# Kernel optimization log

Hardware: AMD Instinct MI355X
Metric: run time of the kernel (lower is better)

The kernel has to match this reference:

```python
import jax, jax.numpy as jnp
import numpy as np

B, S, D_DIM = 32, 512, 1024

def setup_inputs() -> dict:
    key = jax.random.key(0)
    k1, k2, k3, k4 = jax.random.split(key, 4)
    return {
        "D": jax.random.normal(k1, (B, S, D_DIM), dtype=jnp.float32),
        "H": jax.random.normal(k2, (B, S, D_DIM), dtype=jnp.float32),
        # learned params: U is (d+1, d) (xavier-style scale), W is (2d+1,)
        # (original inits W to zeros; we use small random values so the linear
        #  term is exercised — same math either way)
        "U": jax.random.normal(k3, (D_DIM + 1, D_DIM), dtype=jnp.float32) * 0.02,
        "W": jax.random.normal(k4, (2 * D_DIM + 1,), dtype=jnp.float32) * 0.02,
    }

def reference(D, H, U, W):
    # D, H: [B, S, d]; U: [d+1, d]; W: [2d+1]
    d = H.shape[-1]
    ones = jnp.ones(D.shape[:2] + (1,), dtype=D.dtype)
    Daug = jnp.concatenate([D, ones], axis=-1)              # [B, S, d+1]
    # bilinear term: v.U.u  -> [B, Sx, Sy]
    bil = jnp.einsum('bxi,ij,byj->bxy', Daug, U, H)
    # linear term W . concat(D_aug, H): algebraically split — avoids the
    # O(B*S*S*2d) concatenated intermediate of the original implementation
    lin = (Daug @ W[:d + 1])[:, :, None] + (H @ W[d + 1:])[:, None, :]
    return bil + lin
```

## Files before the change

### kernel.cpp

```cpp
#include <hip/hip_runtime.h>


#define D_DIM 1024
#define ROWS 16384

typedef float floatx4 __attribute__((ext_vector_type(4)));
typedef __bf16 bf16x8 __attribute__((ext_vector_type(8)));

__device__ inline unsigned short f2bf(float f) {
  unsigned int u = __builtin_bit_cast(unsigned int, f);
  u = (u + 0x7FFFu + ((u >> 16) & 1u)) >> 16;
  return (unsigned short)u;
}

__device__ inline void async_load16(const void* g, void* l) {
  __builtin_amdgcn_global_load_lds(
      (const __attribute__((address_space(1))) void*)g,
      (__attribute__((address_space(3))) void*)l, 16, 0, 0);
}

__global__ __launch_bounds__(256) void prep_kernel(
    const float* __restrict__ D, const float* __restrict__ H,
    const float* __restrict__ U, const float* __restrict__ W,
    unsigned short* __restrict__ Dbf, unsigned short* __restrict__ Hbf,
    unsigned short* __restrict__ Ut, float* __restrict__ Ubias,
    float* __restrict__ linD) {
  __shared__ float tile[32][33];
  int bid = blockIdx.x;
  int tid = threadIdx.x;
  if (bid < 8192) {
    bool isH = bid >= 4096;
    int wave = tid >> 6, lane = tid & 63;
    int r = ((isH ? bid - 4096 : bid) << 2) + wave;
    const float* src = (isH ? H : D) + (size_t)r * D_DIM;
    unsigned short* dst = (isH ? Hbf : Dbf) + (size_t)r * D_DIM;
    float s = 0.f;
    #pragma unroll
    for (int i = 0; i < 4; ++i) {
      int c = lane + 64 * i;
      float4 v = ((const float4*)src)[c];
      ushort4 o;
      o.x = f2bf(v.x); o.y = f2bf(v.y); o.z = f2bf(v.z); o.w = f2bf(v.w);
      ((ushort4*)dst)[c] = o;
      if (!isH) {
        float4 wv = ((const float4*)W)[c];
        s += v.x * wv.x + v.y * wv.y + v.z * wv.z + v.w * wv.w;
      }
    }
    if (!isH) {
      #pragma unroll
      for (int off = 32; off > 0; off >>= 1) s += __shfl_down(s, off, 64);
      if (lane == 0) linD[r] = s + W[D_DIM];
    }
  } else if (bid < 9216) {
    int t = bid - 8192;
    int n0 = (t & 31) * 32, k0 = (t >> 5) * 32;
    int tr = tid >> 5, tc = tid & 31;
    #pragma unroll
    for (int i = 0; i < 32; i += 8)
      tile[tr + i][tc] = U[(size_t)(k0 + tr + i) * D_DIM + n0 + tc];
    __syncthreads();
    #pragma unroll
    for (int i = 0; i < 32; i += 8)
      Ut[(size_t)(n0 + tr + i) * D_DIM + k0 + tc] = f2bf(tile[tc][tr + i]);
  } else {
    int j = (bid - 9216) * 256 + tid;
    Ubias[j] = U[(size_t)D_DIM * D_DIM + j] + W[D_DIM + 1 + j];
  }
}

__device__ inline void gemm_core_swz(
    const unsigned short* __restrict__ A, const unsigned short* __restrict__ Bt,
    int m0, int n0, unsigned short* As, unsigned short* Bs,
    floatx4 (&acc)[4][4]) {
  const int K = D_DIM;
  int tid = threadIdx.x;
  int l = tid & 63, wave = tid >> 6;
  int quad = l >> 4, lrow = l & 15;
  int wm = wave >> 1, wn = wave & 1;

  int srow = 8 * wave + (l >> 3);
  int sq = (l & 7) ^ (l >> 3);
  const unsigned short* gA = A + (size_t)(m0 + srow) * K + sq * 8;
  const unsigned short* gB = Bt + (size_t)(n0 + srow) * K + sq * 8;

  int rl = lrow & 7, gofs = lrow >> 3;
  int baseA = wm * 512 + gofs * 64 + rl * 8;
  int baseB = wn * 512 + gofs * 64 + rl * 8;

  for (int k0 = 0; k0 < K; k0 += 64) {
    __syncthreads();
    #pragma unroll
    for (int j = 0; j < 4; ++j) {
      async_load16(gA + (size_t)(32 * j) * K + k0, As + (j * 256 + tid) * 8);
      async_load16(gB + (size_t)(32 * j) * K + k0, Bs + (j * 256 + tid) * 8);
    }
    __syncthreads();
    #pragma unroll
    for (int s = 0; s < 2; ++s) {
      int xq = (s * 4 + quad) ^ rl;
      bf16x8 a[4], b[4];
      #pragma unroll
      for (int mt = 0; mt < 4; ++mt)
        a[mt] = *(const bf16x8*)(As + (baseA + mt * 128 + xq) * 8);
      #pragma unroll
      for (int nt = 0; nt < 4; ++nt)
        b[nt] = *(const bf16x8*)(Bs + (baseB + nt * 128 + xq) * 8);
      #pragma unroll
      for (int mt = 0; mt < 4; ++mt)
        #pragma unroll
        for (int nt = 0; nt < 4; ++nt)
          acc[mt][nt] = __builtin_amdgcn_mfma_f32_16x16x32_bf16(
              a[mt], b[nt], acc[mt][nt], 0, 0, 0);
    }
  }
}

__global__ __launch_bounds__(256) void gemm1_kernel(
    const unsigned short* __restrict__ A,
    const unsigned short* __restrict__ Bt,
    const float* __restrict__ Ubias,
    unsigned short* __restrict__ T) {
  __shared__ __align__(16) unsigned short As[128 * 64];
  __shared__ __align__(16) unsigned short Bs[128 * 64];
  int m0 = blockIdx.x * 128, n0 = blockIdx.y * 128;
  int tid = threadIdx.x;
  int lane = tid & 63, wave = tid >> 6;
  int quad = lane >> 4, lrow = lane & 15;
  int wm = wave >> 1, wn = wave & 1;

  floatx4 acc[4][4] = {};
  gemm_core_swz(A, Bt, m0, n0, As, Bs, acc);

  #pragma unroll
  for (int mt = 0; mt < 4; ++mt)
    #pragma unroll
    for (int nt = 0; nt < 4; ++nt) {
      int row = m0 + wm * 64 + mt * 16 + quad * 4;
      int col = n0 + wn * 64 + nt * 16 + lrow;
      float bias = Ubias[col];
      #pragma unroll
      for (int rr = 0; rr < 4; ++rr)
        T[(size_t)(row + rr) * D_DIM + col] = f2bf(acc[mt][nt][rr] + bias);
    }
}

__global__ __launch_bounds__(256) void gemm2_kernel(
    const unsigned short* __restrict__ Tg,
    const unsigned short* __restrict__ Hbf,
    const float* __restrict__ linD,
    float* __restrict__ out) {
  __shared__ __align__(16) unsigned short As[128 * 64];
  __shared__ __align__(16) unsigned short Bs[128 * 64];
  int b = blockIdx.x;
  int t = blockIdx.y;
  int m0 = (t >> 2) * 128, n0 = (t & 3) * 128;
  const unsigned short* A = Tg + (size_t)b * 512 * D_DIM;
  const unsigned short* Bt = Hbf + (size_t)b * 512 * D_DIM;
  int tid = threadIdx.x;
  int lane = tid & 63, wave = tid >> 6;
  int quad = lane >> 4, lrow = lane & 15;
  int wm = wave >> 1, wn = wave & 1;

  floatx4 acc[4][4] = {};
  gemm_core_swz(A, Bt, m0, n0, As, Bs, acc);

  #pragma unroll
  for (int mt = 0; mt < 4; ++mt)
    #pragma unroll
    for (int nt = 0; nt < 4; ++nt) {
      int row = m0 + wm * 64 + mt * 16 + quad * 4;
      int col = n0 + wn * 64 + nt * 16 + lrow;
      #pragma unroll
      for (int rr = 0; rr < 4; ++rr) {
        float v = acc[mt][nt][rr] + linD[b * 512 + row + rr];
        out[((size_t)b * 512 + row + rr) * 512 + col] = v;
      }
    }
}

extern "C" void kernel_launch(void* const* d_in, const int* in_sizes, int n_in,
                              void* d_out, int out_size, void* d_ws, size_t ws_size,
                              hipStream_t stream) {
  const float* D = (const float*)d_in[0];
  const float* H = (const float*)d_in[1];
  const float* U = (const float*)d_in[2];
  const float* W = (const float*)d_in[3];
  float* out = (float*)d_out;

  char* ws = (char*)d_ws;
  unsigned short* Dbf = (unsigned short*)ws; ws += (size_t)ROWS * D_DIM * 2;
  unsigned short* Hbf = (unsigned short*)ws; ws += (size_t)ROWS * D_DIM * 2;
  unsigned short* Tbf = (unsigned short*)ws; ws += (size_t)ROWS * D_DIM * 2;
  unsigned short* Ut  = (unsigned short*)ws; ws += (size_t)D_DIM * D_DIM * 2;
  float* Ubias = (float*)ws;                 ws += (size_t)D_DIM * 4;
  float* linD = (float*)ws;                  ws += (size_t)ROWS * 4;

  prep_kernel<<<dim3(9220), 256, 0, stream>>>(D, H, U, W, Dbf, Hbf, Ut, Ubias, linD);
  gemm1_kernel<<<dim3(128, 8), 256, 0, stream>>>(Dbf, Ut, Ubias, Tbf);
  gemm2_kernel<<<dim3(32, 16), 256, 0, stream>>>(Tbf, Hbf, linD, out);
}
```

Before: 229.4 us.

## Move H bf16 conversion into gemm1 launch to overlap with GEMM work

```diff
diff --git a/kernel.cpp b/kernel.cpp
--- a/kernel.cpp
+++ b/kernel.cpp
@@ -20,40 +20,29 @@
 }
 
 __global__ __launch_bounds__(256) void prep_kernel(
-    const float* __restrict__ D, const float* __restrict__ H,
-    const float* __restrict__ U, const float* __restrict__ W,
-    unsigned short* __restrict__ Dbf, unsigned short* __restrict__ Hbf,
-    unsigned short* __restrict__ Ut, float* __restrict__ Ubias,
-    float* __restrict__ linD) {
+    const float* __restrict__ D, const float* __restrict__ U,
+    const float* __restrict__ W,
+    unsigned short* __restrict__ Dbf, unsigned short* __restrict__ Ut,
+    float* __restrict__ Ubias, float* __restrict__ linD) {
   __shared__ float tile[32][33];
+  __shared__ float red[4];
   int bid = blockIdx.x;
   int tid = threadIdx.x;
-  if (bid < 8192) {
-    bool isH = bid >= 4096;
-    int wave = tid >> 6, lane = tid & 63;
-    int r = ((isH ? bid - 4096 : bid) << 2) + wave;
-    const float* src = (isH ? H : D) + (size_t)r * D_DIM;
-    unsigned short* dst = (isH ? Hbf : Dbf) + (size_t)r * D_DIM;
-    float s = 0.f;
-    #pragma unroll
-    for (int i = 0; i < 4; ++i) {
-      int c = lane + 64 * i;
-      float4 v = ((const float4*)src)[c];
-      ushort4 o;
-      o.x = f2bf(v.x); o.y = f2bf(v.y); o.z = f2bf(v.z); o.w = f2bf(v.w);
-      ((ushort4*)dst)[c] = o;
-      if (!isH) {
-        float4 wv = ((const float4*)W)[c];
-        s += v.x * wv.x + v.y * wv.y + v.z * wv.z + v.w * wv.w;
-      }
-    }
-    if (!isH) {
-      #pragma unroll
-      for (int off = 32; off > 0; off >>= 1) s += __shfl_down(s, off, 64);
-      if (lane == 0) linD[r] = s + W[D_DIM];
-    }
-  } else if (bid < 9216) {
-    int t = bid - 8192;
+  if (bid < ROWS) {
+    const float* src = D + (size_t)bid * D_DIM;
+    float4 v = ((const float4*)src)[tid];
+    float4 wv = ((const float4*)W)[tid];
+    ushort4 o;
+    o.x = f2bf(v.x); o.y = f2bf(v.y); o.z = f2bf(v.z); o.w = f2bf(v.w);
+    ((ushort4*)(Dbf + (size_t)bid * D_DIM))[tid] = o;
+    float s = v.x * wv.x + v.y * wv.y + v.z * wv.z + v.w * wv.w;
+    #pragma unroll
+    for (int off = 32; off > 0; off >>= 1) s += __shfl_down(s, off, 64);
+    if ((tid & 63) == 0) red[tid >> 6] = s;
+    __syncthreads();
+    if (tid == 0) linD[bid] = red[0] + red[1] + red[2] + red[3] + W[D_DIM];
+  } else if (bid < ROWS + 1024) {
+    int t = bid - ROWS;
     int n0 = (t & 31) * 32, k0 = (t >> 5) * 32;
     int tr = tid >> 5, tc = tid & 31;
     #pragma unroll
@@ -64,7 +53,7 @@
     for (int i = 0; i < 32; i += 8)
       Ut[(size_t)(n0 + tr + i) * D_DIM + k0 + tc] = f2bf(tile[tc][tr + i]);
   } else {
-    int j = (bid - 9216) * 256 + tid;
+    int j = (bid - ROWS - 1024) * 256 + tid;
     Ubias[j] = U[(size_t)D_DIM * D_DIM + j] + W[D_DIM + 1 + j];
   }
 }
@@ -120,11 +109,22 @@
     const unsigned short* __restrict__ A,
     const unsigned short* __restrict__ Bt,
     const float* __restrict__ Ubias,
-    unsigned short* __restrict__ T) {
+    unsigned short* __restrict__ T,
+    const float* __restrict__ H,
+    unsigned short* __restrict__ Hbf) {
   __shared__ __align__(16) unsigned short As[128 * 64];
   __shared__ __align__(16) unsigned short Bs[128 * 64];
-  int m0 = blockIdx.x * 128, n0 = blockIdx.y * 128;
-  int tid = threadIdx.x;
+  int bid = blockIdx.x;
+  int tid = threadIdx.x;
+  if (bid >= 1024) {
+    int r = bid - 1024;
+    float4 v = ((const float4*)(H + (size_t)r * D_DIM))[tid];
+    ushort4 o;
+    o.x = f2bf(v.x); o.y = f2bf(v.y); o.z = f2bf(v.z); o.w = f2bf(v.w);
+    ((ushort4*)(Hbf + (size_t)r * D_DIM))[tid] = o;
+    return;
+  }
+  int m0 = (bid & 127) * 128, n0 = (bid >> 7) * 128;
   int lane = tid & 63, wave = tid >> 6;
   int quad = lane >> 4, lrow = lane & 15;
   int wm = wave >> 1, wn = wave & 1;
@@ -196,7 +196,7 @@
   float* Ubias = (float*)ws;                 ws += (size_t)D_DIM * 4;
   float* linD = (float*)ws;                  ws += (size_t)ROWS * 4;
 
-  prep_kernel<<<dim3(9220), 256, 0, stream>>>(D, H, U, W, Dbf, Hbf, Ut, Ubias, linD);
-  gemm1_kernel<<<dim3(128, 8), 256, 0, stream>>>(Dbf, Ut, Ubias, Tbf);
+  prep_kernel<<<dim3(ROWS + 1024 + 4), 256, 0, stream>>>(D, U, W, Dbf, Ut, Ubias, linD);
+  gemm1_kernel<<<dim3(1024 + ROWS), 256, 0, stream>>>(Dbf, Ut, Ubias, Tbf, H, Hbf);
   gemm2_kernel<<<dim3(32, 16), 256, 0, stream>>>(Tbf, Hbf, linD, out);
 }
```

Result: no change. 231.8 us (+1.0%).

## Fuse D/H conversion, both GEMMs into one persistent kernel with per-batch flags

Applied to the files above, without the earlier changes.

```diff
diff --git a/kernel.cpp b/kernel.cpp
--- a/kernel.cpp
+++ b/kernel.cpp
@@ -1,4 +1,5 @@
 #include <hip/hip_runtime.h>
+#include <hip/hip_bf16.h>
 
 
 #define D_DIM 1024
@@ -19,42 +20,23 @@
       (__attribute__((address_space(3))) void*)l, 16, 0, 0);
 }
 
+__device__ inline bf16x8 cvt8(float4 a, float4 b) {
+  union { bf16x8 v; __hip_bfloat162 h[4]; } u;
+  u.h[0] = __float22bfloat162_rn(make_float2(a.x, a.y));
+  u.h[1] = __float22bfloat162_rn(make_float2(a.z, a.w));
+  u.h[2] = __float22bfloat162_rn(make_float2(b.x, b.y));
+  u.h[3] = __float22bfloat162_rn(make_float2(b.z, b.w));
+  return u.v;
+}
+
 __global__ __launch_bounds__(256) void prep_kernel(
-    const float* __restrict__ D, const float* __restrict__ H,
     const float* __restrict__ U, const float* __restrict__ W,
-    unsigned short* __restrict__ Dbf, unsigned short* __restrict__ Hbf,
     unsigned short* __restrict__ Ut, float* __restrict__ Ubias,
-    float* __restrict__ linD) {
+    int* __restrict__ flags) {
   __shared__ float tile[32][33];
-  int bid = blockIdx.x;
-  int tid = threadIdx.x;
-  if (bid < 8192) {
-    bool isH = bid >= 4096;
-    int wave = tid >> 6, lane = tid & 63;
-    int r = ((isH ? bid - 4096 : bid) << 2) + wave;
-    const float* src = (isH ? H : D) + (size_t)r * D_DIM;
-    unsigned short* dst = (isH ? Hbf : Dbf) + (size_t)r * D_DIM;
-    float s = 0.f;
-    #pragma unroll
-    for (int i = 0; i < 4; ++i) {
-      int c = lane + 64 * i;
-      float4 v = ((const float4*)src)[c];
-      ushort4 o;
-      o.x = f2bf(v.x); o.y = f2bf(v.y); o.z = f2bf(v.z); o.w = f2bf(v.w);
-      ((ushort4*)dst)[c] = o;
-      if (!isH) {
-        float4 wv = ((const float4*)W)[c];
-        s += v.x * wv.x + v.y * wv.y + v.z * wv.z + v.w * wv.w;
-      }
-    }
-    if (!isH) {
-      #pragma unroll
-      for (int off = 32; off > 0; off >>= 1) s += __shfl_down(s, off, 64);
-      if (lane == 0) linD[r] = s + W[D_DIM];
-    }
-  } else if (bid < 9216) {
-    int t = bid - 8192;
-    int n0 = (t & 31) * 32, k0 = (t >> 5) * 32;
+  int bid = blockIdx.x, tid = threadIdx.x;
+  if (bid < 1024) {
+    int n0 = (bid & 31) * 32, k0 = (bid >> 5) * 32;
     int tr = tid >> 5, tc = tid & 31;
     #pragma unroll
     for (int i = 0; i < 32; i += 8)
@@ -63,120 +45,213 @@
     #pragma unroll
     for (int i = 0; i < 32; i += 8)
       Ut[(size_t)(n0 + tr + i) * D_DIM + k0 + tc] = f2bf(tile[tc][tr + i]);
+  } else if (bid < 1028) {
+    int j = (bid - 1024) * 256 + tid;
+    Ubias[j] = U[(size_t)D_DIM * D_DIM + j] + W[D_DIM + 1 + j];
   } else {
-    int j = (bid - 9216) * 256 + tid;
-    Ubias[j] = U[(size_t)D_DIM * D_DIM + j] + W[D_DIM + 1 + j];
-  }
-}
-
-__device__ inline void gemm_core_swz(
-    const unsigned short* __restrict__ A, const unsigned short* __restrict__ Bt,
-    int m0, int n0, unsigned short* As, unsigned short* Bs,
-    floatx4 (&acc)[4][4]) {
-  const int K = D_DIM;
-  int tid = threadIdx.x;
-  int l = tid & 63, wave = tid >> 6;
+    if (tid < 32) flags[tid] = 0;
+  }
+}
+
+__device__ inline void stage_u(const unsigned short* __restrict__ Ut,
+                               char* buf, int tid, int it) {
+  int nc = it >> 4, kc = it & 15;
+  #pragma unroll
+  for (int i = 0; i < 4; ++i) {
+    int idx = i * 256 + tid;
+    int nl = idx >> 3, jj = idx & 7, q = jj ^ (nl & 7);
+    async_load16(Ut + (size_t)(nc * 128 + nl) * D_DIM + kc * 64 + q * 8,
+                 buf + idx * 16);
+  }
+}
+
+__device__ inline void stage_2(const unsigned short* __restrict__ Tblk,
+                               const unsigned short* __restrict__ Hbf,
+                               char* buf, int tid, int w, int l, int b, int k2) {
+  #pragma unroll
+  for (int i = 0; i < 2; ++i) {
+    int idx = i * 256 + tid;
+    int m = idx >> 3, jj = idx & 7, q = jj ^ (m & 7);
+    async_load16(Tblk + (size_t)m * D_DIM + k2 * 64 + q * 8, buf + idx * 16);
+  }
+  int q = (l & 7) ^ (l >> 3);
+  #pragma unroll
+  for (int j = 0; j < 16; ++j) {
+    int row = 32 * j + 8 * w + (l >> 3);
+    async_load16(Hbf + ((size_t)b * 512 + row) * D_DIM + k2 * 64 + q * 8,
+                 buf + 8192 + (j * 256 + tid) * 16);
+  }
+}
+
+__global__ __launch_bounds__(256, 1) void fused_kernel(
+    const float* __restrict__ D, const float* __restrict__ H,
+    const float* __restrict__ W, const unsigned short* __restrict__ Ut,
+    const float* __restrict__ Ubias, unsigned short* __restrict__ Hbf,
+    unsigned short* __restrict__ Tbf, float* __restrict__ linDg,
+    int* __restrict__ flags, float* __restrict__ out) {
+  extern __shared__ char smem[];
+  unsigned short* Dls = (unsigned short*)smem;
+  float* linD_lds = (float*)(smem + 131072);
+  char* Ub0 = smem + 131072;
+  char* Ub1 = smem + 147456;
+  int bid = blockIdx.x, tid = threadIdx.x;
+  int b = bid & 31, x = bid >> 5;
+  int l = tid & 63, w = tid >> 6;
   int quad = l >> 4, lrow = l & 15;
-  int wm = wave >> 1, wn = wave & 1;
-
-  int srow = 8 * wave + (l >> 3);
-  int sq = (l & 7) ^ (l >> 3);
-  const unsigned short* gA = A + (size_t)(m0 + srow) * K + sq * 8;
-  const unsigned short* gB = Bt + (size_t)(n0 + srow) * K + sq * 8;
-
-  int rl = lrow & 7, gofs = lrow >> 3;
-  int baseA = wm * 512 + gofs * 64 + rl * 8;
-  int baseB = wn * 512 + gofs * 64 + rl * 8;
-
-  for (int k0 = 0; k0 < K; k0 += 64) {
-    __syncthreads();
-    #pragma unroll
-    for (int j = 0; j < 4; ++j) {
-      async_load16(gA + (size_t)(32 * j) * K + k0, As + (j * 256 + tid) * 8);
-      async_load16(gB + (size_t)(32 * j) * K + k0, Bs + (j * 256 + tid) * 8);
-    }
-    __syncthreads();
+  size_t rowbase = (size_t)b * 512 + x * 64;
+
+  if (tid < 64) linD_lds[tid] = W[D_DIM];
+  __syncthreads();
+  {
+    int q = tid & 127, rh = tid >> 7;
+    float4 w0 = ((const float4*)(W + q * 8))[0];
+    float4 w1 = ((const float4*)(W + q * 8))[1];
+    #pragma unroll 4
+    for (int j = 0; j < 32; ++j) {
+      int row = 2 * j + rh;
+      const float4* src = (const float4*)(D + (rowbase + row) * D_DIM + q * 8);
+      float4 v0 = src[0], v1 = src[1];
+      *(bf16x8*)(Dls + ((size_t)row * 128 + (q ^ (row & 7))) * 8) = cvt8(v0, v1);
+      float s = v0.x * w0.x + v0.y * w0.y + v0.z * w0.z + v0.w * w0.w
+              + v1.x * w1.x + v1.y * w1.y + v1.z * w1.z + v1.w * w1.w;
+      #pragma unroll
+      for (int off = 32; off > 0; off >>= 1) s += __shfl_down(s, off, 64);
+      if (l == 0) atomicAdd(&linD_lds[row], s);
+    }
+    #pragma unroll 4
+    for (int j = 0; j < 32; ++j) {
+      int row = 2 * j + rh;
+      const float4* src = (const float4*)(H + (rowbase + row) * D_DIM + q * 8);
+      float4 v0 = src[0], v1 = src[1];
+      *(bf16x8*)(Hbf + (rowbase + row) * D_DIM + q * 8) = cvt8(v0, v1);
+    }
+  }
+  __threadfence();
+  __syncthreads();
+  if (tid == 0)
+    __hip_atomic_fetch_add(&flags[b], 1, __ATOMIC_RELEASE, __HIP_MEMORY_SCOPE_AGENT);
+  if (tid < 64) linDg[rowbase + tid] = linD_lds[tid];
+  __syncthreads();
+
+  unsigned short* Tblk = Tbf + (size_t)bid * (64 * D_DIM);
+  floatx4 acc[4][2];
+  stage_u(Ut, Ub0, tid, 0);
+  for (int it = 0; it < 128; ++it) {
+    int nc = it >> 4, kc = it & 15;
+    __syncthreads();
+    if (it + 1 < 128) stage_u(Ut, (it & 1) ? Ub0 : Ub1, tid, it + 1);
+    if (kc == 0) {
+      #pragma unroll
+      for (int mt = 0; mt < 4; ++mt)
+        #pragma unroll
+        for (int nt = 0; nt < 2; ++nt)
+          #pragma unroll
+          for (int rr = 0; rr < 4; ++rr) acc[mt][nt][rr] = 0.f;
+    }
+    unsigned short* ub = (unsigned short*)((it & 1) ? Ub1 : Ub0);
     #pragma unroll
     for (int s = 0; s < 2; ++s) {
-      int xq = (s * 4 + quad) ^ rl;
-      bf16x8 a[4], b[4];
+      int qg = kc * 8 + s * 4 + quad;
+      bf16x8 a[4], bb[2];
+      #pragma unroll
+      for (int mt = 0; mt < 4; ++mt) {
+        int m = mt * 16 + lrow;
+        a[mt] = *(const bf16x8*)(Dls + ((size_t)m * 128 + (qg ^ (m & 7))) * 8);
+      }
+      #pragma unroll
+      for (int nt = 0; nt < 2; ++nt) {
+        int nl = w * 32 + nt * 16 + lrow;
+        bb[nt] = *(const bf16x8*)(ub + ((size_t)nl * 8 + ((s * 4 + quad) ^ (nl & 7))) * 8);
+      }
       #pragma unroll
       for (int mt = 0; mt < 4; ++mt)
-        a[mt] = *(const bf16x8*)(As + (baseA + mt * 128 + xq) * 8);
-      #pragma unroll
-      for (int nt = 0; nt < 4; ++nt)
-        b[nt] = *(const bf16x8*)(Bs + (baseB + nt * 128 + xq) * 8);
+        #pragma unroll
+        for (int nt = 0; nt < 2; ++nt)
+          acc[mt][nt] = __builtin_amdgcn_mfma_f32_16x16x32_bf16(
+              a[mt], bb[nt], acc[mt][nt], 0, 0, 0);
+    }
+    if (kc == 15) {
+      #pragma unroll
+      for (int nt = 0; nt < 2; ++nt) {
+        int col = nc * 128 + w * 32 + nt * 16 + lrow;
+        float bias = Ubias[col];
+        #pragma unroll
+        for (int mt = 0; mt < 4; ++mt)
+          #pragma unroll
+          for (int rr = 0; rr < 4; ++rr)
+            Tblk[(size_t)(mt * 16 + quad * 4 + rr) * D_DIM + col] =
+                f2bf(acc[mt][nt][rr] + bias);
+      }
+    }
+  }
+  __syncthreads();
+
+  volatile int* ok = (int*)(smem + 150000);
+  if (tid == 0) {
+    int itc = 0;
+    while (__hip_atomic_load(&flags[b], __ATOMIC_ACQUIRE, __HIP_MEMORY_SCOPE_AGENT) < 8
+           && itc < 20000) { __builtin_amdgcn_s_sleep(8); ++itc; }
+    *ok = (itc < 20000) ? 1 : 0;
+  }
+  __syncthreads();
+  if (!*ok) {
+    int q = tid & 127, rh = tid >> 7;
+    for (int j = 0; j < 256; ++j) {
+      int row = 2 * j + rh;
+      const float4* src = (const float4*)(H + ((size_t)b * 512 + row) * D_DIM + q * 8);
+      float4 v0 = src[0], v1 = src[1];
+      *(bf16x8*)(Hbf + ((size_t)b * 512 + row) * D_DIM + q * 8) = cvt8(v0, v1);
+    }
+    __threadfence();
+    __syncthreads();
+  }
+
+  floatx4 acc2[4][8] = {};
+  char* Sb0 = smem;
+  char* Sb1 = smem + 73728;
+  stage_2(Tblk, Hbf, Sb0, tid, w, l, b, 0);
+  for (int k2 = 0; k2 < 16; ++k2) {
+    __syncthreads();
+    if (k2 + 1 < 16) stage_2(Tblk, Hbf, (k2 & 1) ? Sb0 : Sb1, tid, w, l, b, k2 + 1);
+    unsigned short* tb = (unsigned short*)((k2 & 1) ? Sb1 : Sb0);
+    unsigned short* hb = tb + 4096;
+    #pragma unroll
+    for (int s = 0; s < 2; ++s) {
+      int q = s * 4 + quad;
+      bf16x8 a[4], bb[8];
+      #pragma unroll
+      for (int mt = 0; mt < 4; ++mt) {
+        int m = mt * 16 + lrow;
+        a[mt] = *(const bf16x8*)(tb + ((size_t)m * 8 + (q ^ (m & 7))) * 8);
+      }
+      #pragma unroll
+      for (int yt = 0; yt < 8; ++yt) {
+        int y = w * 128 + yt * 16 + lrow;
+        bb[yt] = *(const bf16x8*)(hb + ((size_t)y * 8 + (q ^ (y & 7))) * 8);
+      }
       #pragma unroll
       for (int mt = 0; mt < 4; ++mt)
         #pragma unroll
-        for (int nt = 0; nt < 4; ++nt)
-          acc[mt][nt] = __builtin_amdgcn_mfma_f32_16x16x32_bf16(
-              a[mt], b[nt], acc[mt][nt], 0, 0, 0);
-    }
-  }
-}
-
-__global__ __launch_bounds__(256) void gemm1_kernel(
-    const unsigned short* __restrict__ A,
-    const unsigned short* __restrict__ Bt,
-    const float* __restrict__ Ubias,
-    unsigned short* __restrict__ T) {
-  __shared__ __align__(16) unsigned short As[128 * 64];
-  __shared__ __align__(16) unsigned short Bs[128 * 64];
-  int m0 = blockIdx.x * 128, n0 = blockIdx.y * 128;
-  int tid = threadIdx.x;
-  int lane = tid & 63, wave = tid >> 6;
-  int quad = lane >> 4, lrow = lane & 15;
-  int wm = wave >> 1, wn = wave & 1;
-
-  floatx4 acc[4][4] = {};
-  gemm_core_swz(A, Bt, m0, n0, As, Bs, acc);
-
-  #pragma unroll
-  for (int mt = 0; mt < 4; ++mt)
-    #pragma unroll
-    for (int nt = 0; nt < 4; ++nt) {
-      int row = m0 + wm * 64 + mt * 16 + quad * 4;
-      int col = n0 + wn * 64 + nt * 16 + lrow;
-      float bias = Ubias[col];
+        for (int yt = 0; yt < 8; ++yt)
+          acc2[mt][yt] = __builtin_amdgcn_mfma_f32_16x16x32_bf16(
+              a[mt], bb[yt], acc2[mt][yt], 0, 0, 0);
+    }
+  }
+  #pragma unroll
+  for (int mt = 0; mt < 4; ++mt) {
+    float ld[4];
+    #pragma unroll
+    for (int rr = 0; rr < 4; ++rr)
+      ld[rr] = linDg[rowbase + mt * 16 + quad * 4 + rr];
+    #pragma unroll
+    for (int yt = 0; yt < 8; ++yt) {
+      int col = w * 128 + yt * 16 + lrow;
       #pragma unroll
       for (int rr = 0; rr < 4; ++rr)
-        T[(size_t)(row + rr) * D_DIM + col] = f2bf(acc[mt][nt][rr] + bias);
-    }
-}
-
-__global__ __launch_bounds__(256) void gemm2_kernel(
-    const unsigned short* __restrict__ Tg,
-    const unsigned short* __restrict__ Hbf,
-    const float* __restrict__ linD,
-    float* __restrict__ out) {
-  __shared__ __align__(16) unsigned short As[128 * 64];
-  __shared__ __align__(16) unsigned short Bs[128 * 64];
-  int b = blockIdx.x;
-  int t = blockIdx.y;
-  int m0 = (t >> 2) * 128, n0 = (t & 3) * 128;
-  const unsigned short* A = Tg + (size_t)b * 512 * D_DIM;
-  const unsigned short* Bt = Hbf + (size_t)b * 512 * D_DIM;
-  int tid = threadIdx.x;
-  int lane = tid & 63, wave = tid >> 6;
-  int quad = lane >> 4, lrow = lane & 15;
-  int wm = wave >> 1, wn = wave & 1;
-
-  floatx4 acc[4][4] = {};
-  gemm_core_swz(A, Bt, m0, n0, As, Bs, acc);
-
-  #pragma unroll
-  for (int mt = 0; mt < 4; ++mt)
-    #pragma unroll
-    for (int nt = 0; nt < 4; ++nt) {
-      int row = m0 + wm * 64 + mt * 16 + quad * 4;
-      int col = n0 + wn * 64 + nt * 16 + lrow;
-      #pragma unroll
-      for (int rr = 0; rr < 4; ++rr) {
-        float v = acc[mt][nt][rr] + linD[b * 512 + row + rr];
-        out[((size_t)b * 512 + row + rr) * 512 + col] = v;
-      }
-    }
+        out[(rowbase + mt * 16 + quad * 4 + rr) * 512 + col] =
+            acc2[mt][yt][rr] + ld[rr];
+    }
+  }
 }
 
 extern "C" void kernel_launch(void* const* d_in, const int* in_sizes, int n_in,
@@ -189,14 +264,16 @@
   float* out = (float*)d_out;
 
   char* ws = (char*)d_ws;
-  unsigned short* Dbf = (unsigned short*)ws; ws += (size_t)ROWS * D_DIM * 2;
   unsigned short* Hbf = (unsigned short*)ws; ws += (size_t)ROWS * D_DIM * 2;
   unsigned short* Tbf = (unsigned short*)ws; ws += (size_t)ROWS * D_DIM * 2;
   unsigned short* Ut  = (unsigned short*)ws; ws += (size_t)D_DIM * D_DIM * 2;
   float* Ubias = (float*)ws;                 ws += (size_t)D_DIM * 4;
-  float* linD = (float*)ws;                  ws += (size_t)ROWS * 4;
-
-  prep_kernel<<<dim3(9220), 256, 0, stream>>>(D, H, U, W, Dbf, Hbf, Ut, Ubias, linD);
-  gemm1_kernel<<<dim3(128, 8), 256, 0, stream>>>(Dbf, Ut, Ubias, Tbf);
-  gemm2_kernel<<<dim3(32, 16), 256, 0, stream>>>(Tbf, Hbf, linD, out);
-}
+  float* linDg = (float*)ws;                 ws += (size_t)ROWS * 4;
+  int* flags   = (int*)ws;                   ws += 128;
+
+  prep_kernel<<<dim3(1029), 256, 0, stream>>>(U, W, Ut, Ubias, flags);
+  hipFuncSetAttribute((const void*)fused_kernel,
+                      hipFuncAttributeMaxDynamicSharedMemorySize, 163840);
+  fused_kernel<<<dim3(256), 256, 163840, stream>>>(
+      D, H, W, Ut, Ubias, Hbf, Tbf, linDg, flags, out);
+}
```

After: 323.7 us. 1.41x slower.

## Double-buffer LDS tiles in GEMM core and restructure bf16 prep kernel

Applied to the files above, without the earlier changes.

```diff
diff --git a/kernel.cpp b/kernel.cpp
--- a/kernel.cpp
+++ b/kernel.cpp
@@ -11,6 +11,12 @@
   unsigned int u = __builtin_bit_cast(unsigned int, f);
   u = (u + 0x7FFFu + ((u >> 16) & 1u)) >> 16;
   return (unsigned short)u;
+}
+
+__device__ inline ushort4 cvt4(float4 v) {
+  ushort4 o;
+  o.x = f2bf(v.x); o.y = f2bf(v.y); o.z = f2bf(v.z); o.w = f2bf(v.w);
+  return o;
 }
 
 __device__ inline void async_load16(const void* g, void* l) {
@@ -26,31 +32,33 @@
     unsigned short* __restrict__ Ut, float* __restrict__ Ubias,
     float* __restrict__ linD) {
   __shared__ float tile[32][33];
-  int bid = blockIdx.x;
-  int tid = threadIdx.x;
+  int bid = blockIdx.x, tid = threadIdx.x;
   if (bid < 8192) {
-    bool isH = bid >= 4096;
-    int wave = tid >> 6, lane = tid & 63;
-    int r = ((isH ? bid - 4096 : bid) << 2) + wave;
-    const float* src = (isH ? H : D) + (size_t)r * D_DIM;
-    unsigned short* dst = (isH ? Hbf : Dbf) + (size_t)r * D_DIM;
-    float s = 0.f;
-    #pragma unroll
-    for (int i = 0; i < 4; ++i) {
-      int c = lane + 64 * i;
-      float4 v = ((const float4*)src)[c];
-      ushort4 o;
-      o.x = f2bf(v.x); o.y = f2bf(v.y); o.z = f2bf(v.z); o.w = f2bf(v.w);
-      ((ushort4*)dst)[c] = o;
-      if (!isH) {
-        float4 wv = ((const float4*)W)[c];
-        s += v.x * wv.x + v.y * wv.y + v.z * wv.z + v.w * wv.w;
-      }
-    }
+    int w = tid >> 6, l = tid & 63;
+    bool isH = w >= 2;
+    int row = 2 * bid + (w & 1);
+    const float* src = (isH ? H : D) + (size_t)row * D_DIM;
+    float4 v0 = ((const float4*)src)[l];
+    float4 v1 = ((const float4*)src)[l + 64];
+    float4 v2 = ((const float4*)src)[l + 128];
+    float4 v3 = ((const float4*)src)[l + 192];
+    unsigned short* dst = (isH ? Hbf : Dbf) + (size_t)row * D_DIM;
+    ((ushort4*)dst)[l]       = cvt4(v0);
+    ((ushort4*)dst)[l + 64]  = cvt4(v1);
+    ((ushort4*)dst)[l + 128] = cvt4(v2);
+    ((ushort4*)dst)[l + 192] = cvt4(v3);
     if (!isH) {
+      float4 w0 = ((const float4*)W)[l];
+      float4 w1 = ((const float4*)W)[l + 64];
+      float4 w2 = ((const float4*)W)[l + 128];
+      float4 w3 = ((const float4*)W)[l + 192];
+      float s = v0.x*w0.x + v0.y*w0.y + v0.z*w0.z + v0.w*w0.w
+              + v1.x*w1.x + v1.y*w1.y + v1.z*w1.z + v1.w*w1.w
+              + v2.x*w2.x + v2.y*w2.y + v2.z*w2.z + v2.w*w2.w
+              + v3.x*w3.x + v3.y*w3.y + v3.z*w3.z + v3.w*w3.w;
       #pragma unroll
       for (int off = 32; off > 0; off >>= 1) s += __shfl_down(s, off, 64);
-      if (lane == 0) linD[r] = s + W[D_DIM];
+      if (l == 0) linD[row] = s + W[D_DIM];
     }
   } else if (bid < 9216) {
     int t = bid - 8192;
@@ -69,10 +77,20 @@
   }
 }
 
-__device__ inline void gemm_core_swz(
+__device__ inline void stage_tile(const unsigned short* gA, const unsigned short* gB,
+                                  int k0, unsigned short* Ab, unsigned short* Bb,
+                                  int tid) {
+  #pragma unroll
+  for (int j = 0; j < 4; ++j) {
+    async_load16(gA + (size_t)(32 * j) * D_DIM + k0, Ab + (j * 256 + tid) * 8);
+    async_load16(gB + (size_t)(32 * j) * D_DIM + k0, Bb + (j * 256 + tid) * 8);
+  }
+}
+
+__device__ inline void gemm_core_dbuf(
     const unsigned short* __restrict__ A, const unsigned short* __restrict__ Bt,
-    int m0, int n0, unsigned short* As, unsigned short* Bs,
-    floatx4 (&acc)[4][4]) {
+    int m0, int n0, unsigned short* As0, unsigned short* Bs0,
+    unsigned short* As1, unsigned short* Bs1, floatx4 (&acc)[4][4]) {
   const int K = D_DIM;
   int tid = threadIdx.x;
   int l = tid & 63, wave = tid >> 6;
@@ -88,24 +106,24 @@
   int baseA = wm * 512 + gofs * 64 + rl * 8;
   int baseB = wn * 512 + gofs * 64 + rl * 8;
 
+  stage_tile(gA, gB, 0, As0, Bs0, tid);
   for (int k0 = 0; k0 < K; k0 += 64) {
+    int par = (k0 >> 6) & 1;
+    unsigned short* Ac = par ? As1 : As0;
+    unsigned short* Bc = par ? Bs1 : Bs0;
     __syncthreads();
-    #pragma unroll
-    for (int j = 0; j < 4; ++j) {
-      async_load16(gA + (size_t)(32 * j) * K + k0, As + (j * 256 + tid) * 8);
-      async_load16(gB + (size_t)(32 * j) * K + k0, Bs + (j * 256 + tid) * 8);
-    }
-    __syncthreads();
+    if (k0 + 64 < K)
+      stage_tile(gA, gB, k0 + 64, par ? As0 : As1, par ? Bs0 : Bs1, tid);
     #pragma unroll
     for (int s = 0; s < 2; ++s) {
       int xq = (s * 4 + quad) ^ rl;
       bf16x8 a[4], b[4];
       #pragma unroll
       for (int mt = 0; mt < 4; ++mt)
-        a[mt] = *(const bf16x8*)(As + (baseA + mt * 128 + xq) * 8);
+        a[mt] = *(const bf16x8*)(Ac + (baseA + mt * 128 + xq) * 8);
       #pragma unroll
       for (int nt = 0; nt < 4; ++nt)
-        b[nt] = *(const bf16x8*)(Bs + (baseB + nt * 128 + xq) * 8);
+        b[nt] = *(const bf16x8*)(Bc + (baseB + nt * 128 + xq) * 8);
       #pragma unroll
       for (int mt = 0; mt < 4; ++mt)
         #pragma unroll
@@ -121,8 +139,10 @@
     const unsigned short* __restrict__ Bt,
     const float* __restrict__ Ubias,
     unsigned short* __restrict__ T) {
-  __shared__ __align__(16) unsigned short As[128 * 64];
-  __shared__ __align__(16) unsigned short Bs[128 * 64];
+  __shared__ __align__(16) unsigned short As0[128 * 64];
+  __shared__ __align__(16) unsigned short Bs0[128 * 64];
+  __shared__ __align__(16) unsigned short As1[128 * 64];
+  __shared__ __align__(16) unsigned short Bs1[128 * 64];
   int m0 = blockIdx.x * 128, n0 = blockIdx.y * 128;
   int tid = threadIdx.x;
   int lane = tid & 63, wave = tid >> 6;
@@ -130,7 +150,7 @@
   int wm = wave >> 1, wn = wave & 1;
 
   floatx4 acc[4][4] = {};
-  gemm_core_swz(A, Bt, m0, n0, As, Bs, acc);
+  gemm_core_dbuf(A, Bt, m0, n0, As0, Bs0, As1, Bs1, acc);
 
   #pragma unroll
   for (int mt = 0; mt < 4; ++mt)
@@ -150,8 +170,10 @@
     const unsigned short* __restrict__ Hbf,
     const float* __restrict__ linD,
     float* __restrict__ out) {
-  __shared__ __align__(16) unsigned short As[128 * 64];
-  __shared__ __align__(16) unsigned short Bs[128 * 64];
+  __shared__ __align__(16) unsigned short As0[128 * 64];
+  __shared__ __align__(16) unsigned short Bs0[128 * 64];
+  __shared__ __align__(16) unsigned short As1[128 * 64];
+  __shared__ __align__(16) unsigned short Bs1[128 * 64];
   int b = blockIdx.x;
   int t = blockIdx.y;
   int m0 = (t >> 2) * 128, n0 = (t & 3) * 128;
@@ -163,7 +185,7 @@
   int wm = wave >> 1, wn = wave & 1;
 
   floatx4 acc[4][4] = {};
-  gemm_core_swz(A, Bt, m0, n0, As, Bs, acc);
+  gemm_core_dbuf(A, Bt, m0, n0, As0, Bs0, As1, Bs1, acc);
 
   #pragma unroll
   for (int mt = 0; mt < 4; ++mt)
@@ -194,7 +216,7 @@
   unsigned short* Tbf = (unsigned short*)ws; ws += (size_t)ROWS * D_DIM * 2;
   unsigned short* Ut  = (unsigned short*)ws; ws += (size_t)D_DIM * D_DIM * 2;
   float* Ubias = (float*)ws;                 ws += (size_t)D_DIM * 4;
-  float* linD = (float*)ws;                  ws += (size_t)ROWS * 4;
+  float* linD  = (float*)ws;                 ws += (size_t)ROWS * 4;
 
   prep_kernel<<<dim3(9220), 256, 0, stream>>>(D, H, U, W, Dbf, Hbf, Ut, Ubias, linD);
   gemm1_kernel<<<dim3(128, 8), 256, 0, stream>>>(Dbf, Ut, Ubias, Tbf);
```

Result: no change. 226.0 us (-1.5%).
